# Kernel tuning notes

Hardware: AMD Instinct MI355X
Metric: run time of the kernel (lower is better)

The kernel has to match this reference:

```python
import jax, jax.numpy as jnp
import numpy as np


def setup_inputs() -> dict:
    key = jax.random.key(0)
    k1, k2 = jax.random.split(key)
    B, d = 4096, 1023
    S = 2 * d + 1  # 2047
    predictions = jax.random.normal(k1, (B, S, 2), dtype=jnp.float32)
    targets = jax.random.normal(k2, (B, S, 2), dtype=jnp.float32)
    return {"predictions": predictions, "targets": targets, "d": d, "batch_size": B}


def reference(predictions, targets, d, batch_size):
    # Sum of squared differences over batch, the first 2*d+1 positions,
    # and both (x, y) coordinates; normalized by (2d+1) and batch_size.
    S = 2 * d + 1
    diff = predictions[:batch_size, :S, :2] - targets[:batch_size, :S, :2]
    total = jnp.sum(diff * diff)
    return total / S / batch_size
```

## Files before the change

kernel.cpp:

```cpp
#include <hip/hip_runtime.h>

__global__ __launch_bounds__(256, 4) void ssd_partials(const float4* __restrict__ p,
                                                       const float4* __restrict__ t,
                                                       float* __restrict__ ws,
                                                       int n4) {
    const int tid = threadIdx.x;
    const int stride = gridDim.x * 256;
    int i = blockIdx.x * 256 + tid;

    float acc0 = 0.f, acc1 = 0.f, acc2 = 0.f, acc3 = 0.f;
    for (; i < n4; i += stride) {
        float4 a = p[i];
        float4 b = t[i];
        float dx = a.x - b.x; acc0 += dx * dx;
        float dy = a.y - b.y; acc1 += dy * dy;
        float dz = a.z - b.z; acc2 += dz * dz;
        float dw = a.w - b.w; acc3 += dw * dw;
    }
    float acc = (acc0 + acc1) + (acc2 + acc3);

    #pragma unroll
    for (int off = 32; off > 0; off >>= 1)
        acc += __shfl_down(acc, off, 64);

    __shared__ float wave_sums[4];
    const int lane = tid & 63;
    const int wave = tid >> 6;
    if (lane == 0) wave_sums[wave] = acc;
    __syncthreads();

    if (tid == 0)
        ws[blockIdx.x] = (wave_sums[0] + wave_sums[1]) + (wave_sums[2] + wave_sums[3]);
}

__global__ __launch_bounds__(256) void ssd_finalize(const float* __restrict__ ws,
                                                    float* __restrict__ out,
                                                    float scale) {
    const int tid = threadIdx.x;
    float acc = 0.f;
    #pragma unroll
    for (int k = 0; k < 8; ++k) {
        int idx = tid + k * 256;
        if (idx < 2047) acc += ws[idx];
    }

    #pragma unroll
    for (int off = 32; off > 0; off >>= 1)
        acc += __shfl_down(acc, off, 64);

    __shared__ float wave_sums[4];
    const int lane = tid & 63;
    const int wave = tid >> 6;
    if (lane == 0) wave_sums[wave] = acc;
    __syncthreads();

    if (tid == 0)
        out[0] = ((wave_sums[0] + wave_sums[1]) + (wave_sums[2] + wave_sums[3])) * scale;
}

extern "C" void kernel_launch(void* const* d_in, const int* in_sizes, int n_in,
                              void* d_out, int out_size, void* d_ws, size_t ws_size,
                              hipStream_t stream) {
    const float* pred = (const float*)d_in[0];
    const float* targ = (const float*)d_in[1];
    float* out = (float*)d_out;
    float* ws = (float*)d_ws;

    const int B = 4096;
    const int S = 2047;
    const float scale = 1.0f / ((float)S * (float)B);
    const int n4 = B * S * 2 / 4;

    ssd_partials<<<2047, 256, 0, stream>>>((const float4*)pred,
                                           (const float4*)targ, ws, n4);
    ssd_finalize<<<1, 256, 0, stream>>>(ws, out, scale);
}
```

Baseline: 150.2 us.

## Stream inputs through LDS with async global_load_lds triple buffering

Replaces the grid-stride register loads with asynchronous global-to-LDS DMA loads (global_load_lds, 16 bytes per lane) into a three-stage shared buffer. Each iteration issues the next stage's loads and then waits on vmcnt before reading the current stage from LDS. The trip count is fixed at 8, which relies on n4 = 2047*256*8 exactly, and the bounds check is dropped. This trades a round trip through LDS and manual waitcnt encoding for deeper overlap of memory latency.

Measured after the change: 148.6 us. No clear change (-1.1%).

```diff
diff --git a/kernel.cpp b/kernel.cpp
--- a/kernel.cpp
+++ b/kernel.cpp
@@ -2,16 +2,40 @@
 
 __global__ __launch_bounds__(256, 4) void ssd_partials(const float4* __restrict__ p,
                                                        const float4* __restrict__ t,
-                                                       float* __restrict__ ws,
-                                                       int n4) {
-    const int tid = threadIdx.x;
-    const int stride = gridDim.x * 256;
-    int i = blockIdx.x * 256 + tid;
+                                                       float* __restrict__ ws) {
+    const int tid  = threadIdx.x;
+    const int lane = tid & 63;
+    const int wave = tid >> 6;
+    const long long stride = 2047LL * 256;
+    const long long i0 = (long long)blockIdx.x * 256 + tid;
+
+    __shared__ float4 st[3][2][4][64];
+
+    typedef const __attribute__((address_space(1))) float gfloat;
+    typedef __attribute__((address_space(3))) float lfloat;
+
+    const float4* gp = p + i0;
+    const float4* gt = t + i0;
+
+    __builtin_amdgcn_global_load_lds((gfloat*)gp, (lfloat*)&st[0][0][wave][0], 16, 0, 0);
+    __builtin_amdgcn_global_load_lds((gfloat*)gt, (lfloat*)&st[0][1][wave][0], 16, 0, 0);
 
     float acc0 = 0.f, acc1 = 0.f, acc2 = 0.f, acc3 = 0.f;
-    for (; i < n4; i += stride) {
-        float4 a = p[i];
-        float4 b = t[i];
+    #pragma unroll
+    for (int k = 0; k < 8; ++k) {
+        if (k < 7) {
+            __builtin_amdgcn_global_load_lds((gfloat*)(gp + (k + 1) * stride),
+                                             (lfloat*)&st[(k + 1) % 3][0][wave][0], 16, 0, 0);
+            __builtin_amdgcn_global_load_lds((gfloat*)(gt + (k + 1) * stride),
+                                             (lfloat*)&st[(k + 1) % 3][1][wave][0], 16, 0, 0);
+            __builtin_amdgcn_s_waitcnt(0xF72);
+        } else {
+            __builtin_amdgcn_s_waitcnt(0xF70);
+        }
+        __builtin_amdgcn_sched_barrier(0);
+
+        float4 a = st[k % 3][0][wave][lane];
+        float4 b = st[k % 3][1][wave][lane];
         float dx = a.x - b.x; acc0 += dx * dx;
         float dy = a.y - b.y; acc1 += dy * dy;
         float dz = a.z - b.z; acc2 += dz * dz;
@@ -24,8 +48,6 @@
         acc += __shfl_down(acc, off, 64);
 
     __shared__ float wave_sums[4];
-    const int lane = tid & 63;
-    const int wave = tid >> 6;
     if (lane == 0) wave_sums[wave] = acc;
     __syncthreads();
 
@@ -69,9 +91,8 @@
     const int B = 4096;
     const int S = 2047;
     const float scale = 1.0f / ((float)S * (float)B);
-    const int n4 = B * S * 2 / 4;
 
     ssd_partials<<<2047, 256, 0, stream>>>((const float4*)pred,
-                                           (const float4*)targ, ws, n4);
+                                           (const float4*)targ, ws);
     ssd_finalize<<<1, 256, 0, stream>>>(ws, out, scale);
 }
```
